# Performance work log

Measured on AMD Instinct MI355X. Metric: run time of the kernel, lower is better.

Reference implementation:

```python
import jax, jax.numpy as jnp
import numpy as np

H, M = 1024, 8
HM = H * M
DT, TM, TA, TZI, TZJ, TP = 0.001, 0.05, 2.7, 0.24, 0.24, 10.0
EPS = np.float32(np.finfo(np.float32).tiny)


def log_eps(x):
    return jnp.log(jnp.where(x <= 0.0, EPS, x))


def setup_inputs() -> dict:
    key = jax.random.key(0)
    ks = jax.random.split(key, 13)
    f32 = jnp.float32
    return {
        "x": jax.random.uniform(ks[0], (H, M), f32),
        "s": jax.random.normal(ks[1], (H, M), f32),
        "o": jax.random.uniform(ks[2], (H, M), f32),
        "a": jax.random.normal(ks[3], (H, M), f32) * 0.1,
        "zi": jax.random.uniform(ks[4], (H, M), f32),
        "zj": jax.random.uniform(ks[5], (H, M), f32),
        "p": jax.random.uniform(ks[6], (), f32),
        "pi": jax.random.uniform(ks[7], (H, M), f32),
        "pj": jax.random.uniform(ks[8], (H, M), f32),
        "pij": jax.random.uniform(ks[9], (HM, HM), f32),
        "b": jax.random.normal(ks[10], (H, M), f32),
        "w": jax.random.normal(ks[11], (HM, HM), f32) * 0.01,
        "noise": jax.random.normal(ks[12], (H, M), f32),
        "ga": jnp.float32(1.0),
        "gw": jnp.float32(1.0),
        "gb": jnp.float32(1.0),
        "gs": jnp.float32(0.1),
        "k": jnp.float32(1.0),
    }


def reference(x, s, o, a, zi, zj, p, pi, pj, pij, b, w, noise, ga, gw, gb, gs, k):
    # --- update_state (train=True uses gw) ---
    st = gw * (b.reshape(-1) + w.T @ o.reshape(-1))          # GEMV, [HM]
    s_new = s + DT / TM * (st.reshape(H, M) - a + log_eps(x) + gs * noise - s)
    o_new = jax.nn.softmax(s_new, axis=1)
    a_new = a + DT / TA * (ga * o_new - a)
    # --- update_traces ---
    zi_new = zi + DT / TZI * (o_new - zi)
    zj_new = zj + DT / TZJ * (o_new - zj)
    # --- update_probabilities ---
    c = k * DT / TP
    p_new = p + c * (1.0 - p)
    pi_new = pi + c * (zi_new - pi)
    pj_new = pj + c * (zj_new - pj)
    pij_new = pij + c * (jnp.outer(zi_new.reshape(-1), zj_new.reshape(-1)) - pij)
    # --- update_connections ---
    w_new = log_eps(p_new * pij_new / jnp.outer(pi_new.reshape(-1), pj_new.reshape(-1)))
    b_new = gb * log_eps(pj_new)
    # torch forward returns o (buffers updated in place); JAX returns full new state
    return (o_new, s_new, a_new, zi_new, zj_new, p_new, pi_new, pj_new, pij_new, w_new, b_new)
```

## Files before the change

### kernel.cpp

```cpp
#include <hip/hip_runtime.h>
#include <math.h>

#define H_N 1024
#define M_N 8
#define HM 8192
#define NIC 64

typedef float f32x4 __attribute__((ext_vector_type(4)));

static __device__ __forceinline__ float log_eps(float x) {
    const float EPS_TINY = 1.17549435e-38f;
    return __logf(x <= 0.0f ? EPS_TINY : x);
}

__global__ __launch_bounds__(256) void gemv_partial(const float* __restrict__ w,
                                                    const float* __restrict__ o,
                                                    float* __restrict__ pbuf) {
    const int jb = blockIdx.x & 7;
    const int ic = blockIdx.x >> 3;
    const int j0 = jb * 1024 + threadIdx.x * 4;
    const int i0 = ic * 128;
    f32x4 acc = {0.f, 0.f, 0.f, 0.f};
    const float* wp = w + (size_t)i0 * HM + j0;
#pragma unroll 4
    for (int i = 0; i < 128; ++i) {
        const float ov = o[i0 + i];
        const f32x4 wv = *reinterpret_cast<const f32x4*>(wp);
        acc.x += wv.x * ov; acc.y += wv.y * ov; acc.z += wv.z * ov; acc.w += wv.w * ov;
        wp += HM;
    }
    *reinterpret_cast<f32x4*>(&pbuf[(size_t)ic * HM + j0]) = acc;
}

__global__ __launch_bounds__(256) void row_kernel(
    const float* __restrict__ x, const float* __restrict__ s,
    const float* __restrict__ a, const float* __restrict__ zi,
    const float* __restrict__ zj, const float* __restrict__ p,
    const float* __restrict__ pi, const float* __restrict__ pj,
    const float* __restrict__ b, const float* __restrict__ noise,
    const float* __restrict__ ga, const float* __restrict__ gw,
    const float* __restrict__ gb, const float* __restrict__ gs,
    const float* __restrict__ k, const float* __restrict__ pbuf,
    float* __restrict__ out) {
    const int r = blockIdx.x * blockDim.x + threadIdx.x;
    if (r >= H_N) return;

    const float gwv = gw[0], gav = ga[0], gbv = gb[0], gsv = gs[0], kv = k[0], pv = p[0];
    const float c = kv * 1e-4f;

    float* o_new  = out;
    float* s_new  = out + (size_t)HM;
    float* a_new  = out + (size_t)2 * HM;
    float* zi_new = out + (size_t)3 * HM;
    float* zj_new = out + (size_t)4 * HM;
    float* p_new  = out + (size_t)5 * HM;
    float* pi_new = out + (size_t)5 * HM + 1;
    float* pj_new = out + (size_t)6 * HM + 1;
    float* b_new  = out + (size_t)7 * HM + 1 + (size_t)2 * HM * HM;

    const int base = r * M_N;

    f32x4 r0 = {0.f, 0.f, 0.f, 0.f}, r1 = {0.f, 0.f, 0.f, 0.f};
#pragma unroll 8
    for (int ic = 0; ic < NIC; ++ic) {
        const float* pp = pbuf + (size_t)ic * HM + base;
        const f32x4 v0 = *reinterpret_cast<const f32x4*>(pp);
        const f32x4 v1 = *reinterpret_cast<const f32x4*>(pp + 4);
        r0.x += v0.x; r0.y += v0.y; r0.z += v0.z; r0.w += v0.w;
        r1.x += v1.x; r1.y += v1.y; r1.z += v1.z; r1.w += v1.w;
    }
    const float stv[M_N] = {r0.x, r0.y, r0.z, r0.w, r1.x, r1.y, r1.z, r1.w};

    float sv[M_N], ev[M_N];
    float mx = -3.0e38f;
#pragma unroll
    for (int m = 0; m < M_N; ++m) {
        const int i = base + m;
        const float st = gwv * (b[i] + stv[m]);
        const float sn = s[i] + 0.02f * (st - a[i] + log_eps(x[i]) + gsv * noise[i] - s[i]);
        sv[m] = sn;
        mx = fmaxf(mx, sn);
    }
    float sum = 0.f;
#pragma unroll
    for (int m = 0; m < M_N; ++m) { ev[m] = __expf(sv[m] - mx); sum += ev[m]; }
    const float rs = 1.0f / sum;
#pragma unroll
    for (int m = 0; m < M_N; ++m) {
        const int i = base + m;
        const float on  = ev[m] * rs;
        const float an  = a[i]  + (float)(0.001 / 2.7)  * (gav * on - a[i]);
        const float zin = zi[i] + (float)(0.001 / 0.24) * (on - zi[i]);
        const float zjn = zj[i] + (float)(0.001 / 0.24) * (on - zj[i]);
        const float pin = pi[i] + c * (zin - pi[i]);
        const float pjn = pj[i] + c * (zjn - pj[i]);
        o_new[i]  = on;
        s_new[i]  = sv[m];
        a_new[i]  = an;
        zi_new[i] = zin;
        zj_new[i] = zjn;
        pi_new[i] = pin;
        pj_new[i] = pjn;
        b_new[i]  = gbv * log_eps(pjn);
    }
    if (r == 0) p_new[0] = pv + c * (1.0f - pv);
}

__global__ __launch_bounds__(256) void outer_kernel(
    const float* __restrict__ pij, const float* __restrict__ out_ro,
    float* __restrict__ out, const float* __restrict__ p,
    const float* __restrict__ k) {
    const float* zi_new = out_ro + (size_t)3 * HM;
    const float* zj_new = out_ro + (size_t)4 * HM;
    const float* pi_new = out_ro + (size_t)5 * HM + 1;
    const float* pj_new = out_ro + (size_t)6 * HM + 1;
    float* pij_new = out + (size_t)7 * HM + 1;
    float* w_new   = pij_new + (size_t)HM * HM;

    const float kv = k[0], pv = p[0];
    const float c  = kv * 1e-4f;
    const float pn = pv + c * (1.0f - pv);

    const size_t nvec   = (size_t)HM * HM / 4;
    const size_t stride = (size_t)gridDim.x * blockDim.x;
    for (size_t v = (size_t)blockIdx.x * blockDim.x + threadIdx.x; v < nvec; v += stride) {
        const size_t idx = v * 4;
        const int I = (int)(idx >> 13);
        const int J = (int)(idx & 8191);
        const float ziI = zi_new[I];
        const float piI = pi_new[I];
        const f32x4 pv4 = *reinterpret_cast<const f32x4*>(&pij[idx]);
        const float zj0 = zj_new[J + 0], zj1 = zj_new[J + 1], zj2 = zj_new[J + 2], zj3 = zj_new[J + 3];
        const float pj0 = pj_new[J + 0], pj1 = pj_new[J + 1], pj2 = pj_new[J + 2], pj3 = pj_new[J + 3];

        const float q0 = pv4.x + c * (ziI * zj0 - pv4.x);
        const float q1 = pv4.y + c * (ziI * zj1 - pv4.y);
        const float q2 = pv4.z + c * (ziI * zj2 - pv4.z);
        const float q3 = pv4.w + c * (ziI * zj3 - pv4.w);

        pij_new[idx + 0] = q0;
        pij_new[idx + 1] = q1;
        pij_new[idx + 2] = q2;
        pij_new[idx + 3] = q3;

        const float v0 = __fdividef(pn * q0, piI * pj0);
        const float v1 = __fdividef(pn * q1, piI * pj1);
        const float v2 = __fdividef(pn * q2, piI * pj2);
        const float v3 = __fdividef(pn * q3, piI * pj3);

        w_new[idx + 0] = log_eps(v0);
        w_new[idx + 1] = log_eps(v1);
        w_new[idx + 2] = log_eps(v2);
        w_new[idx + 3] = log_eps(v3);
    }
}

extern "C" void kernel_launch(void* const* d_in, const int* in_sizes, int n_in,
                              void* d_out, int out_size, void* d_ws, size_t ws_size,
                              hipStream_t stream) {
    const float* x     = (const float*)d_in[0];
    const float* s     = (const float*)d_in[1];
    const float* o     = (const float*)d_in[2];
    const float* a     = (const float*)d_in[3];
    const float* zi    = (const float*)d_in[4];
    const float* zj    = (const float*)d_in[5];
    const float* p     = (const float*)d_in[6];
    const float* pi    = (const float*)d_in[7];
    const float* pj    = (const float*)d_in[8];
    const float* pij   = (const float*)d_in[9];
    const float* b     = (const float*)d_in[10];
    const float* w     = (const float*)d_in[11];
    const float* noise = (const float*)d_in[12];
    const float* ga    = (const float*)d_in[13];
    const float* gw    = (const float*)d_in[14];
    const float* gb    = (const float*)d_in[15];
    const float* gs    = (const float*)d_in[16];
    const float* k     = (const float*)d_in[17];

    float* out  = (float*)d_out;
    float* pbuf = (float*)d_ws;

    gemv_partial<<<512, 256, 0, stream>>>(w, o, pbuf);
    row_kernel<<<(H_N + 255) / 256, 256, 0, stream>>>(
        x, s, a, zi, zj, p, pi, pj, b, noise, ga, gw, gb, gs, k, pbuf, out);
    outer_kernel<<<2048, 256, 0, stream>>>(pij, out, out, p, k);
}
```

Baseline: 262.1 us.

## Widen GEMV split-K and parallelize row kernel per element with shuffle softmax

Result: slower. 279.2 us (+6.5%).

```diff
diff --git a/kernel.cpp b/kernel.cpp
--- a/kernel.cpp
+++ b/kernel.cpp
@@ -4,7 +4,6 @@
 #define H_N 1024
 #define M_N 8
 #define HM 8192
-#define NIC 64
 
 typedef float f32x4 __attribute__((ext_vector_type(4)));
 
@@ -15,15 +14,16 @@
 
 __global__ __launch_bounds__(256) void gemv_partial(const float* __restrict__ w,
                                                     const float* __restrict__ o,
-                                                    float* __restrict__ pbuf) {
+                                                    float* __restrict__ pbuf,
+                                                    int rows_per_chunk) {
     const int jb = blockIdx.x & 7;
     const int ic = blockIdx.x >> 3;
     const int j0 = jb * 1024 + threadIdx.x * 4;
-    const int i0 = ic * 128;
+    const int i0 = ic * rows_per_chunk;
     f32x4 acc = {0.f, 0.f, 0.f, 0.f};
     const float* wp = w + (size_t)i0 * HM + j0;
 #pragma unroll 4
-    for (int i = 0; i < 128; ++i) {
+    for (int i = 0; i < rows_per_chunk; ++i) {
         const float ov = o[i0 + i];
         const f32x4 wv = *reinterpret_cast<const f32x4*>(wp);
         acc.x += wv.x * ov; acc.y += wv.y * ov; acc.z += wv.z * ov; acc.w += wv.w * ov;
@@ -41,9 +41,9 @@
     const float* __restrict__ ga, const float* __restrict__ gw,
     const float* __restrict__ gb, const float* __restrict__ gs,
     const float* __restrict__ k, const float* __restrict__ pbuf,
-    float* __restrict__ out) {
-    const int r = blockIdx.x * blockDim.x + threadIdx.x;
-    if (r >= H_N) return;
+    int nic, float* __restrict__ out) {
+    const int j = blockIdx.x * blockDim.x + threadIdx.x;
+    if (j >= HM) return;
 
     const float gwv = gw[0], gav = ga[0], gbv = gb[0], gsv = gs[0], kv = k[0], pv = p[0];
     const float c = kv * 1e-4f;
@@ -58,52 +58,39 @@
     float* pj_new = out + (size_t)6 * HM + 1;
     float* b_new  = out + (size_t)7 * HM + 1 + (size_t)2 * HM * HM;
 
-    const int base = r * M_N;
+    float st = 0.f;
+#pragma unroll 8
+    for (int ic = 0; ic < nic; ++ic) st += pbuf[(size_t)ic * HM + j];
 
-    f32x4 r0 = {0.f, 0.f, 0.f, 0.f}, r1 = {0.f, 0.f, 0.f, 0.f};
-#pragma unroll 8
-    for (int ic = 0; ic < NIC; ++ic) {
-        const float* pp = pbuf + (size_t)ic * HM + base;
-        const f32x4 v0 = *reinterpret_cast<const f32x4*>(pp);
-        const f32x4 v1 = *reinterpret_cast<const f32x4*>(pp + 4);
-        r0.x += v0.x; r0.y += v0.y; r0.z += v0.z; r0.w += v0.w;
-        r1.x += v1.x; r1.y += v1.y; r1.z += v1.z; r1.w += v1.w;
-    }
-    const float stv[M_N] = {r0.x, r0.y, r0.z, r0.w, r1.x, r1.y, r1.z, r1.w};
+    const float stv = gwv * (b[j] + st);
+    const float sn  = s[j] + 0.02f * (stv - a[j] + log_eps(x[j]) + gsv * noise[j] - s[j]);
 
-    float sv[M_N], ev[M_N];
-    float mx = -3.0e38f;
-#pragma unroll
-    for (int m = 0; m < M_N; ++m) {
-        const int i = base + m;
-        const float st = gwv * (b[i] + stv[m]);
-        const float sn = s[i] + 0.02f * (st - a[i] + log_eps(x[i]) + gsv * noise[i] - s[i]);
-        sv[m] = sn;
-        mx = fmaxf(mx, sn);
-    }
-    float sum = 0.f;
-#pragma unroll
-    for (int m = 0; m < M_N; ++m) { ev[m] = __expf(sv[m] - mx); sum += ev[m]; }
-    const float rs = 1.0f / sum;
-#pragma unroll
-    for (int m = 0; m < M_N; ++m) {
-        const int i = base + m;
-        const float on  = ev[m] * rs;
-        const float an  = a[i]  + (float)(0.001 / 2.7)  * (gav * on - a[i]);
-        const float zin = zi[i] + (float)(0.001 / 0.24) * (on - zi[i]);
-        const float zjn = zj[i] + (float)(0.001 / 0.24) * (on - zj[i]);
-        const float pin = pi[i] + c * (zin - pi[i]);
-        const float pjn = pj[i] + c * (zjn - pj[i]);
-        o_new[i]  = on;
-        s_new[i]  = sv[m];
-        a_new[i]  = an;
-        zi_new[i] = zin;
-        zj_new[i] = zjn;
-        pi_new[i] = pin;
-        pj_new[i] = pjn;
-        b_new[i]  = gbv * log_eps(pjn);
-    }
-    if (r == 0) p_new[0] = pv + c * (1.0f - pv);
+    float mx = sn;
+    mx = fmaxf(mx, __shfl_xor(mx, 1));
+    mx = fmaxf(mx, __shfl_xor(mx, 2));
+    mx = fmaxf(mx, __shfl_xor(mx, 4));
+    const float e = __expf(sn - mx);
+    float sum = e;
+    sum += __shfl_xor(sum, 1);
+    sum += __shfl_xor(sum, 2);
+    sum += __shfl_xor(sum, 4);
+    const float on = e / sum;
+
+    const float an  = a[j]  + (float)(0.001 / 2.7)  * (gav * on - a[j]);
+    const float zin = zi[j] + (float)(0.001 / 0.24) * (on - zi[j]);
+    const float zjn = zj[j] + (float)(0.001 / 0.24) * (on - zj[j]);
+    const float pin = pi[j] + c * (zin - pi[j]);
+    const float pjn = pj[j] + c * (zjn - pj[j]);
+
+    o_new[j]  = on;
+    s_new[j]  = sn;
+    a_new[j]  = an;
+    zi_new[j] = zin;
+    zj_new[j] = zjn;
+    pi_new[j] = pin;
+    pj_new[j] = pjn;
+    b_new[j]  = gbv * log_eps(pjn);
+    if (j == 0) p_new[0] = pv + c * (1.0f - pv);
 }
 
 __global__ __launch_bounds__(256) void outer_kernel(
@@ -123,6 +110,7 @@
 
     const size_t nvec   = (size_t)HM * HM / 4;
     const size_t stride = (size_t)gridDim.x * blockDim.x;
+#pragma unroll 2
     for (size_t v = (size_t)blockIdx.x * blockDim.x + threadIdx.x; v < nvec; v += stride) {
         const size_t idx = v * 4;
         const int I = (int)(idx >> 13);
@@ -180,8 +168,14 @@
     float* out  = (float*)d_out;
     float* pbuf = (float*)d_ws;
 
-    gemv_partial<<<512, 256, 0, stream>>>(w, o, pbuf);
-    row_kernel<<<(H_N + 255) / 256, 256, 0, stream>>>(
-        x, s, a, zi, zj, p, pi, pj, b, noise, ga, gw, gb, gs, k, pbuf, out);
+    int nic;
+    if      (ws_size >= (size_t)256 * HM * sizeof(float)) nic = 256;
+    else if (ws_size >= (size_t)128 * HM * sizeof(float)) nic = 128;
+    else                                                  nic = 64;
+    const int rpc = HM / nic;
+
+    gemv_partial<<<8 * nic, 256, 0, stream>>>(w, o, pbuf, rpc);
+    row_kernel<<<HM / 256, 256, 0, stream>>>(
+        x, s, a, zi, zj, p, pi, pj, b, noise, ga, gw, gb, gs, k, pbuf, nic, out);
     outer_kernel<<<2048, 256, 0, stream>>>(pij, out, out, p, k);
 }
```

## Restructure GEMV to stream contiguous rows and reduce via atomic slices

Applied to the files above, without the earlier changes.

After: 318.4 us. 1.21x slower.

```diff
diff --git a/kernel.cpp b/kernel.cpp
--- a/kernel.cpp
+++ b/kernel.cpp
@@ -4,7 +4,7 @@
 #define H_N 1024
 #define M_N 8
 #define HM 8192
-#define NIC 64
+#define NSL 8
 
 typedef float f32x4 __attribute__((ext_vector_type(4)));
 
@@ -13,23 +13,30 @@
     return __logf(x <= 0.0f ? EPS_TINY : x);
 }
 
-__global__ __launch_bounds__(256) void gemv_partial(const float* __restrict__ w,
+__global__ __launch_bounds__(256) void gemv_stream2(const float* __restrict__ w,
                                                     const float* __restrict__ o,
                                                     float* __restrict__ pbuf) {
-    const int jb = blockIdx.x & 7;
-    const int ic = blockIdx.x >> 3;
-    const int j0 = jb * 1024 + threadIdx.x * 4;
-    const int i0 = ic * 128;
-    f32x4 acc = {0.f, 0.f, 0.f, 0.f};
-    const float* wp = w + (size_t)i0 * HM + j0;
-#pragma unroll 4
-    for (int i = 0; i < 128; ++i) {
+    const int b  = blockIdx.x;
+    const int i0 = b * 16;
+    const int t4 = threadIdx.x * 4;
+    f32x4 acc[8] = {};
+    for (int i = 0; i < 16; ++i) {
         const float ov = o[i0 + i];
-        const f32x4 wv = *reinterpret_cast<const f32x4*>(wp);
-        acc.x += wv.x * ov; acc.y += wv.y * ov; acc.z += wv.z * ov; acc.w += wv.w * ov;
-        wp += HM;
+        const float* rp = w + (size_t)(i0 + i) * HM + t4;
+#pragma unroll
+        for (int p8 = 0; p8 < 8; ++p8) {
+            const f32x4 wv = *reinterpret_cast<const f32x4*>(rp + p8 * 1024);
+            acc[p8] += wv * ov;
+        }
     }
-    *reinterpret_cast<f32x4*>(&pbuf[(size_t)ic * HM + j0]) = acc;
+    float* pb = pbuf + (size_t)(b & (NSL - 1)) * HM + t4;
+#pragma unroll
+    for (int p8 = 0; p8 < 8; ++p8) {
+        atomicAdd(&pb[p8 * 1024 + 0], acc[p8].x);
+        atomicAdd(&pb[p8 * 1024 + 1], acc[p8].y);
+        atomicAdd(&pb[p8 * 1024 + 2], acc[p8].z);
+        atomicAdd(&pb[p8 * 1024 + 3], acc[p8].w);
+    }
 }
 
 __global__ __launch_bounds__(256) void row_kernel(
@@ -61,13 +68,13 @@
     const int base = r * M_N;
 
     f32x4 r0 = {0.f, 0.f, 0.f, 0.f}, r1 = {0.f, 0.f, 0.f, 0.f};
-#pragma unroll 8
-    for (int ic = 0; ic < NIC; ++ic) {
-        const float* pp = pbuf + (size_t)ic * HM + base;
+#pragma unroll
+    for (int sl = 0; sl < NSL; ++sl) {
+        const float* pp = pbuf + (size_t)sl * HM + base;
         const f32x4 v0 = *reinterpret_cast<const f32x4*>(pp);
         const f32x4 v1 = *reinterpret_cast<const f32x4*>(pp + 4);
-        r0.x += v0.x; r0.y += v0.y; r0.z += v0.z; r0.w += v0.w;
-        r1.x += v1.x; r1.y += v1.y; r1.z += v1.z; r1.w += v1.w;
+        r0 += v0;
+        r1 += v1;
     }
     const float stv[M_N] = {r0.x, r0.y, r0.z, r0.w, r1.x, r1.y, r1.z, r1.w};
 
@@ -180,7 +187,8 @@
     float* out  = (float*)d_out;
     float* pbuf = (float*)d_ws;
 
-    gemv_partial<<<512, 256, 0, stream>>>(w, o, pbuf);
+    (void)hipMemsetAsync(pbuf, 0, (size_t)NSL * HM * sizeof(float), stream);
+    gemv_stream2<<<512, 256, 0, stream>>>(w, o, pbuf);
     row_kernel<<<(H_N + 255) / 256, 256, 0, stream>>>(
         x, s, a, zi, zj, p, pi, pj, b, noise, ga, gw, gb, gs, k, pbuf, out);
     outer_kernel<<<2048, 256, 0, stream>>>(pij, out, out, p, k);
```
